# Kernel tuning notes

Hardware: AMD Instinct MI355X
Metric: run time of the kernel (lower is better)

Reference implementation:

```python
import jax, jax.numpy as jnp
import numpy as np

REG_MAX = 16
NC = 80
TOPK = 10
ALPHA = 0.5
BETA = 6.0
IMG = 640.0
EPS = 1e-7
BOX_W, CLS_W, DFL_W = 7.5, 0.5, 1.5


def make_anchors():
    anchors, strides = [], []
    for s, size in [(8, 80), (16, 40), (32, 20)]:
        yy, xx = jnp.meshgrid(jnp.arange(size, dtype=jnp.float32), jnp.arange(size, dtype=jnp.float32), indexing='ij')
        xy = (jnp.stack([xx, yy], -1).reshape(-1, 2) + 0.5) * s
        anchors.append(xy)
        strides.append(jnp.full((size * size,), float(s), jnp.float32))
    return jnp.concatenate(anchors), jnp.concatenate(strides)  # [A,2], [A]


def pairwise_iou(gt, pd, eps=EPS):
    # gt [B,G,4], pd [B,A,4] -> [B,G,A]
    b1 = gt[:, :, None, :]
    b2 = pd[:, None, :, :]
    inter = jnp.clip(jnp.minimum(b1[..., 2:], b2[..., 2:]) - jnp.maximum(b1[..., :2], b2[..., :2]), 0.0).prod(-1)
    a1 = (b1[..., 2:] - b1[..., :2]).prod(-1)
    a2 = (b2[..., 2:] - b2[..., :2]).prod(-1)
    return inter / (a1 + a2 - inter + eps)


def ciou(b1, b2, eps=EPS):
    # elementwise CIoU on [...,4] xyxy boxes
    inter = jnp.clip(jnp.minimum(b1[..., 2:], b2[..., 2:]) - jnp.maximum(b1[..., :2], b2[..., :2]), 0.0).prod(-1)
    area1 = jnp.maximum(b1[..., 2:] - b1[..., :2], eps).prod(-1)
    area2 = jnp.maximum(b2[..., 2:] - b2[..., :2], eps).prod(-1)
    union = area1 + area2 - inter + eps
    iou = inter / union
    cw = jnp.maximum(b1[..., 2], b2[..., 2]) - jnp.minimum(b1[..., 0], b2[..., 0])
    ch = jnp.maximum(b1[..., 3], b2[..., 3]) - jnp.minimum(b1[..., 1], b2[..., 1])
    c2 = cw * cw + ch * ch + eps
    c1c = (b1[..., :2] + b1[..., 2:]) * 0.5
    c2c = (b2[..., :2] + b2[..., 2:]) * 0.5
    rho2 = ((c1c - c2c) ** 2).sum(-1)
    w1 = jnp.maximum(b1[..., 2] - b1[..., 0], eps)
    h1 = jnp.maximum(b1[..., 3] - b1[..., 1], eps)
    w2 = jnp.maximum(b2[..., 2] - b2[..., 0], eps)
    h2 = jnp.maximum(b2[..., 3] - b2[..., 1], eps)
    v = (4.0 / jnp.pi ** 2) * (jnp.arctan(w2 / h2) - jnp.arctan(w1 / h1)) ** 2
    alpha = jax.lax.stop_gradient(v / (1.0 - iou + v + eps))
    return jnp.clip(iou - (rho2 / c2 + v * alpha), -1.0, 1.0)


def assign(pd_scores, pd_bboxes, gt_labels, gt_bboxes, mask_gt_f):
    # TaskAlignedAssigner.forward (runs under stop_gradient at call site)
    B, A, C = pd_scores.shape
    G = gt_bboxes.shape[1]
    iou = pairwise_iou(gt_bboxes, pd_bboxes)                       # [B,G,A]
    cls_score = pd_scores.max(-1)[:, None, :] * mask_gt_f[:, :, None]
    align = (cls_score ** ALPHA) * (iou ** BETA) * mask_gt_f[:, :, None]
    k = min(TOPK, A)
    vals, idx = jax.lax.top_k(align, k)                            # [B,G,k]
    valid = (mask_gt_f[:, :, None] > 0) & (vals > 0)
    b_ix = jnp.arange(B)[:, None, None]
    g_ix = jnp.arange(G)[None, :, None]
    mask_pos = jnp.zeros((B, G, A), bool).at[b_ix, g_ix, idx].max(valid)
    fg = mask_pos.any(1)                                           # [B,A]
    miou = iou * mask_pos.astype(iou.dtype)
    matched = miou.argmax(1)                                       # [B,A]
    tlab = jnp.take_along_axis(gt_labels, matched, 1)
    tlab = jnp.clip(tlab, 0, C - 1)
    tlab = jnp.where(fg, tlab, 0)
    tbox = jnp.take_along_axis(gt_bboxes, matched[..., None], 1)   # [B,A,4]
    iou_s = jnp.take_along_axis(miou, matched[:, None, :], 1)[:, 0, :]
    tscore = jax.nn.one_hot(tlab, C, dtype=pd_scores.dtype) * iou_s[..., None] * fg[..., None].astype(pd_scores.dtype)
    return tlab, tbox, tscore, fg


def yolo_loss(pred_dist, pred_cls, gt_labels, gt_bboxes, mask_gt):
    B, A, _ = pred_dist.shape
    R = REG_MAX
    anchors, strides = make_anchors()
    # decode: DFL expectation -> pixel boxes
    prob = jax.nn.softmax(pred_dist.reshape(B, A, 4, R), -1)
    dist = (prob * jnp.arange(R, dtype=prob.dtype)).sum(-1)        # stride units
    dpix = dist * strides[None, :, None]
    ax, ay = anchors[None, :, 0], anchors[None, :, 1]
    pred_boxes = jnp.clip(jnp.stack([ax - dpix[..., 0], ay - dpix[..., 1], ax + dpix[..., 2], ay + dpix[..., 3]], -1), 0.0, IMG)
    pd_scores = jax.nn.sigmoid(pred_cls)
    mgf = mask_gt.astype(jnp.float32)
    tlab, tbox, tscore, fg = jax.tree.map(jax.lax.stop_gradient, assign(pd_scores, pred_boxes, gt_labels, gt_bboxes, mgf))
    # cls: BCE with logits, sum / max(score_sum, 1)
    x, t = pred_cls, tscore
    bce = jnp.maximum(x, 0.0) - x * t + jnp.log1p(jnp.exp(-jnp.abs(x)))
    score_sum = jnp.maximum(tscore.sum(), 1.0)
    loss_cls = bce.sum() / score_sum
    fgf = fg.astype(jnp.float32)
    num_fg = jnp.maximum(fgf.sum(), 1.0)
    # box: mean(1 - CIoU) over foreground anchors
    loss_box = ((1.0 - ciou(pred_boxes, tbox)) * fgf).sum() / num_fg
    # DFL: box2dist in stride units, bilinear CE over left/right bins
    target_ltrb = jnp.stack([ax - tbox[..., 0], ay - tbox[..., 1], tbox[..., 2] - ax, tbox[..., 3] - ay], -1) / strides[None, :, None]
    target_ltrb = jnp.clip(target_ltrb, 0.0, R - 1.01)
    tleft = jnp.clip(jnp.floor(target_ltrb).astype(jnp.int32), 0, R - 1)
    tright = jnp.clip(tleft + 1, 0, R - 1)
    wr = jnp.clip(target_ltrb - tleft.astype(target_ltrb.dtype), 0.0, 1.0)
    wl = 1.0 - wr
    logp = jax.nn.log_softmax(pred_dist.reshape(B, A, 4, R), -1)
    ll = -jnp.take_along_axis(logp, tleft[..., None], -1)[..., 0]
    lr = -jnp.take_along_axis(logp, tright[..., None], -1)[..., 0]
    dfl = (ll * wl + lr * wr).sum(-1)                              # [B,A]
    loss_dfl = (dfl * fgf).sum() / num_fg / 4.0
    return BOX_W * loss_box + CLS_W * loss_cls + DFL_W * loss_dfl


def setup_inputs() -> dict:
    key = jax.random.key(0)
    k0, k1, k2, k3, k4 = jax.random.split(key, 5)
    B, A, G = 32, 8400, 40
    pred_dist = jax.random.normal(k0, (B, A, 4 * REG_MAX), dtype=jnp.float32)
    pred_cls = jax.random.normal(k1, (B, A, NC), dtype=jnp.float32)
    gt_labels = jax.random.randint(k2, (B, G), 0, NC)
    centers = jax.random.uniform(k3, (B, G, 2), minval=60.0, maxval=580.0)
    wh = jax.random.uniform(k4, (B, G, 2), minval=10.0, maxval=100.0)
    gt_bboxes = jnp.concatenate([centers - wh * 0.5, centers + wh * 0.5], -1).astype(jnp.float32)
    mask_gt = jnp.ones((B, G), dtype=bool)
    return {"pred_dist": pred_dist, "pred_cls": pred_cls, "gt_labels": gt_labels, "gt_bboxes": gt_bboxes, "mask_gt": mask_gt}


def reference(pred_dist, pred_cls, gt_labels, gt_bboxes, mask_gt):
    return yolo_loss(pred_dist, pred_cls, gt_labels, gt_bboxes, mask_gt)
```

## Files before the change

kernel.cpp:

```cpp
#include <hip/hip_runtime.h>
#include <cmath>


namespace {

constexpr int B = 32;
constexpr int A = 8400;
constexpr int G = 40;
constexpr int C = 80;
constexpr float EPS = 1e-7f;
constexpr float IMG = 640.0f;

constexpr int TPW = 16;
constexpr int NT = B * A / TPW;
constexpr int PRE_BLOCKS = 512;
constexpr int NWAVES = PRE_BLOCKS * 4;
constexpr int DIST_B = TPW * 64;
constexpr int CLS_B = TPW * 320;
constexpr int SLICE = DIST_B + CLS_B;

#define AS1 __attribute__((address_space(1)))
#define AS3 __attribute__((address_space(3)))

__device__ __forceinline__ void gload_lds16(const void* g, void* l) {
  __builtin_amdgcn_global_load_lds((AS1 void*)(g), (AS3 void*)(l), 16, 0, 0);
}

__device__ __forceinline__ void anchor_of(int a, float& ax, float& ay, float& st) {
  int x, y;
  if (a < 6400)      { x = a % 80; y = a / 80; st = 8.0f; }
  else if (a < 8000) { int t = a - 6400; x = t % 40; y = t / 40; st = 16.0f; }
  else               { int t = a - 8000; x = t % 20; y = t / 20; st = 32.0f; }
  ax = ((float)x + 0.5f) * st;
  ay = ((float)y + 0.5f) * st;
}

__device__ __forceinline__ void cls_part(const float4* c, float& sp, float& mx) {
  float relu = 0.f, p0 = 1.f, p1 = 1.f;
  mx = -3.4e38f;
#pragma unroll
  for (int q = 0; q < 5; ++q) {
    float xs[4] = {c[q].x, c[q].y, c[q].z, c[q].w};
#pragma unroll
    for (int e = 0; e < 4; ++e) {
      float x = xs[e];
      mx = fmaxf(mx, x);
      relu += fmaxf(x, 0.f);
      float ee = __expf(-fabsf(x));
      if (q < 3) p0 *= (1.f + ee); else p1 *= (1.f + ee);
    }
  }
  sp = relu + 0.69314718056f * (__log2f(p0) + __log2f(p1));
}

__device__ __forceinline__ float dist_expect(float4 w0, float4 w1, float4 w2, float4 w3) {
  float x[16] = {w0.x, w0.y, w0.z, w0.w, w1.x, w1.y, w1.z, w1.w,
                 w2.x, w2.y, w2.z, w2.w, w3.x, w3.y, w3.z, w3.w};
  float m = x[0];
#pragma unroll
  for (int e = 1; e < 16; ++e) m = fmaxf(m, x[e]);
  float se = 0.f, sj = 0.f;
#pragma unroll
  for (int e = 0; e < 16; ++e) {
    float ee = __expf(x[e] - m);
    se += ee;
    sj += ee * (float)e;
  }
  return sj / se;
}

__device__ __forceinline__ void stage_tile(const char* dbase, const char* cbase,
                                           int tile, char* lbuf, int lane) {
  const char* gd = dbase + (size_t)tile * DIST_B + lane * 16;
  const char* gc = cbase + (size_t)tile * CLS_B + lane * 16;
#pragma unroll
  for (int r = 0; r < 4; ++r) gload_lds16(gd + r * 1024, lbuf + r * 1024);
#pragma unroll
  for (int q = 0; q < 5; ++q) gload_lds16(gc + q * 1024, lbuf + DIST_B + q * 1024);
}

__global__ __launch_bounds__(256) void k_pre(
    const float* __restrict__ pred_dist, const float* __restrict__ pred_cls,
    float* __restrict__ pbox, float* __restrict__ msqrt,
    unsigned long long* __restrict__ mask, double* __restrict__ acc) {
  __shared__ char smem[4 * 2 * SLICE];
  __shared__ double shb[4];
  int t = threadIdx.x, lane = t & 63, wid = t >> 6;
  int j = lane & 3, a16 = lane >> 2;
  char* slice = smem + wid * (2 * SLICE);
  const char* dbase = (const char*)pred_dist;
  const char* cbase = (const char*)pred_cls;

  double spsum = 0.0;
  int cur = blockIdx.x * 4 + wid;
  int buf = 0;
  if (cur < NT) stage_tile(dbase, cbase, cur, slice, lane);

  while (cur < NT) {
    int nxt = cur + NWAVES;
    if (nxt < NT) {
      stage_tile(dbase, cbase, nxt, slice + (buf ^ 1) * SLICE, lane);
      __builtin_amdgcn_s_waitcnt(0xF79);
    } else {
      __builtin_amdgcn_s_waitcnt(0xF70);
    }

    const char* bp = slice + buf * SLICE;
    float4 c[5];
    const float4* cl = (const float4*)(bp + DIST_B + a16 * 320 + j * 16);
#pragma unroll
    for (int q = 0; q < 5; ++q) c[q] = cl[q * 4];
    float sp, mx;
    cls_part(c, sp, mx);
    mx = fmaxf(mx, __shfl_xor(mx, 1));
    mx = fmaxf(mx, __shfl_xor(mx, 2));

    const float4* dl = (const float4*)(bp + a16 * 256 + j * 64);
    float de = dist_expect(dl[0], dl[1], dl[2], dl[3]);
    int qb = lane & ~3;
    float e0 = __shfl(de, qb), e1 = __shfl(de, qb + 1);
    float e2 = __shfl(de, qb + 2), e3 = __shfl(de, qb + 3);

    int i = cur * TPW + a16;
    if (j == 0) {
      int a = i % A;
      float ax, ay, st;
      anchor_of(a, ax, ay, st);
      float4 ob;
      ob.x = fminf(fmaxf(ax - e0 * st, 0.f), IMG);
      ob.y = fminf(fmaxf(ay - e1 * st, 0.f), IMG);
      ob.z = fminf(fmaxf(ax + e2 * st, 0.f), IMG);
      ob.w = fminf(fmaxf(ay + e3 * st, 0.f), IMG);
      reinterpret_cast<float4*>(pbox)[i] = ob;
      msqrt[i] = sqrtf(1.f / (1.f + __expf(-mx)));
      mask[i] = 0ull;
    }
    spsum += (double)sp;
    cur = nxt;
    buf ^= 1;
  }

#pragma unroll
  for (int off = 32; off; off >>= 1) spsum += __shfl_xor(spsum, off);
  if (lane == 0) shb[wid] = spsum;
  __syncthreads();
  if (t == 0) {
    double s = shb[0] + shb[1] + shb[2] + shb[3];
    atomicAdd(&acc[0 * 8 + (blockIdx.x & 7)], s);
  }
}

__global__ __launch_bounds__(256) void k_topk(
    const float* __restrict__ pbox, const float* __restrict__ msqrt,
    const float* __restrict__ gt_bboxes, unsigned long long* __restrict__ mask) {
  int bg = blockIdx.x;
  int b = bg / G, g = bg % G;
  int t = threadIdx.x, lane = t & 63, wid = t >> 6;
  const float* gp = gt_bboxes + (size_t)bg * 4;
  float gx1 = gp[0], gy1 = gp[1], gx2 = gp[2], gy2 = gp[3];
  float garea = (gx2 - gx1) * (gy2 - gy1);
  const float4* pb = reinterpret_cast<const float4*>(pbox) + (size_t)b * A;
  const float* ms = msqrt + (size_t)b * A;

  float lv[10];
  int li[10];
#pragma unroll
  for (int s = 0; s < 10; ++s) { lv[s] = 0.f; li[s] = 0x7fffffff; }

  for (int a = t; a < A; a += 256) {
    float4 p = pb[a];
    float iw = fmaxf(fminf(gx2, p.z) - fmaxf(gx1, p.x), 0.f);
    float ih = fmaxf(fminf(gy2, p.w) - fmaxf(gy1, p.y), 0.f);
    float inter = iw * ih;
    float parea = (p.z - p.x) * (p.w - p.y);
    float iou = inter / (garea + parea - inter + EPS);
    float i2 = iou * iou;
    float v = ms[a] * i2 * i2 * i2;
    if (v > lv[9] || (v == lv[9] && v > 0.f && a < li[9])) {
      float cv = v; int ci = a;
#pragma unroll
      for (int s = 0; s < 10; ++s) {
        bool bt = (cv > lv[s]) || (cv == lv[s] && ci < li[s]);
        float tv = bt ? cv : lv[s]; int ti = bt ? ci : li[s];
        cv = bt ? lv[s] : cv; ci = bt ? li[s] : ci;
        lv[s] = tv; li[s] = ti;
      }
    }
  }

  __shared__ float swv[4];
  __shared__ int swi[4];
  __shared__ float sbv;
  __shared__ int sbi;
  int ptr = 0;
  unsigned long long* mrow = mask + (size_t)b * A;
  for (int k = 0; k < 10; ++k) {
    float hv = lv[0]; int hi = li[0];
#pragma unroll
    for (int s = 1; s < 10; ++s) { bool sel = (ptr == s); hv = sel ? lv[s] : hv; hi = sel ? li[s] : hi; }
    if (ptr > 9) { hv = -1.f; hi = -1; }
    float rv = hv; int ri = hi;
#pragma unroll
    for (int off = 32; off; off >>= 1) {
      float ov = __shfl_xor(rv, off); int oi = __shfl_xor(ri, off);
      if (ov > rv || (ov == rv && oi < ri)) { rv = ov; ri = oi; }
    }
    if (lane == 0) { swv[wid] = rv; swi[wid] = ri; }
    __syncthreads();
    if (t == 0) {
      float bv = swv[0]; int bi = swi[0];
#pragma unroll
      for (int w = 1; w < 4; ++w)
        if (swv[w] > bv || (swv[w] == bv && swi[w] < bi)) { bv = swv[w]; bi = swi[w]; }
      sbv = bv; sbi = bi;
      if (bv > 0.f) atomicOr(&mrow[bi], 1ull << g);
    }
    __syncthreads();
    if (sbv <= 0.f) break;
    if (hi == sbi) ptr++;
  }
}

__device__ __forceinline__ float ciou_f(float4 p, float t0, float t1, float t2, float t3) {
  float iw = fmaxf(fminf(p.z, t2) - fmaxf(p.x, t0), 0.f);
  float ih = fmaxf(fminf(p.w, t3) - fmaxf(p.y, t1), 0.f);
  float inter = iw * ih;
  float w1 = fmaxf(p.z - p.x, EPS), h1 = fmaxf(p.w - p.y, EPS);
  float w2 = fmaxf(t2 - t0, EPS), h2 = fmaxf(t3 - t1, EPS);
  float uni = w1 * h1 + w2 * h2 - inter + EPS;
  float iou = inter / uni;
  float cw = fmaxf(p.z, t2) - fminf(p.x, t0);
  float ch = fmaxf(p.w, t3) - fminf(p.y, t1);
  float c2 = cw * cw + ch * ch + EPS;
  float dx = (p.x + p.z) * 0.5f - (t0 + t2) * 0.5f;
  float dy = (p.y + p.w) * 0.5f - (t1 + t3) * 0.5f;
  float rho2 = dx * dx + dy * dy;
  float dat = atanf(w2 / h2) - atanf(w1 / h1);
  const float c4pi2 = (float)(4.0 / (M_PI * M_PI));
  float v = c4pi2 * dat * dat;
  float alpha = v / (1.0f - iou + v + EPS);
  float r = iou - (rho2 / c2 + v * alpha);
  return fminf(fmaxf(r, -1.f), 1.f);
}

__device__ __forceinline__ float wave_sum(float v) {
#pragma unroll
  for (int off = 32; off; off >>= 1) v += __shfl_xor(v, off);
  return v;
}

__global__ __launch_bounds__(256) void k_loss(
    const float* __restrict__ pred_dist, const float* __restrict__ pred_cls,
    const int* __restrict__ gt_labels, const float* __restrict__ gt_bboxes,
    const float* __restrict__ pbox, const unsigned long long* __restrict__ mask,
    double* __restrict__ acc) {
  int t = threadIdx.x, lane = t & 63, wid = t >> 6;
  int i = blockIdx.x * 256 + t;
  int b = i / A, a = i - b * A;
  unsigned long long mk = mask[i];
  float corr = 0.f, sc = 0.f, nfg = 0.f, box = 0.f, dfl = 0.f;
  if (mk) {
    float4 p = reinterpret_cast<const float4*>(pbox)[i];
    float parea = (p.z - p.x) * (p.w - p.y);
    float best = 0.f;
    int bestg = -1;
    unsigned long long mm = mk;
    while (mm) {
      int g = __ffsll((unsigned long long)mm) - 1;
      mm &= mm - 1;
      const float* gp = gt_bboxes + (size_t)(b * G + g) * 4;
      float gx1 = gp[0], gy1 = gp[1], gx2 = gp[2], gy2 = gp[3];
      float iw = fmaxf(fminf(gx2, p.z) - fmaxf(gx1, p.x), 0.f);
      float ih = fmaxf(fminf(gy2, p.w) - fmaxf(gy1, p.y), 0.f);
      float inter = iw * ih;
      float garea = (gx2 - gx1) * (gy2 - gy1);
      float iou = inter / (garea + parea - inter + EPS);
      if (iou > best) { best = iou; bestg = g; }
    }
    if (bestg >= 0) {
      sc = best;
      nfg = 1.f;
      int lab = gt_labels[b * G + bestg];
      lab = lab < 0 ? 0 : (lab > C - 1 ? C - 1 : lab);
      float xl = pred_cls[(size_t)i * C + lab];
      corr = -xl * best;
      const float* gp = gt_bboxes + (size_t)(b * G + bestg) * 4;
      float t0 = gp[0], t1 = gp[1], t2 = gp[2], t3 = gp[3];
      box = 1.0f - ciou_f(p, t0, t1, t2, t3);
      float ax, ay, st;
      anchor_of(a, ax, ay, st);
      float rst = 1.f / st;
      float tgt[4] = {(ax - t0) * rst, (ay - t1) * rst, (t2 - ax) * rst, (t3 - ay) * rst};
      const float4* dr = reinterpret_cast<const float4*>(pred_dist) + (size_t)i * 16;
      const float* drf = pred_dist + (size_t)i * 64;
#pragma unroll
      for (int l = 0; l < 4; ++l) {
        float4 u0 = dr[4 * l], u1 = dr[4 * l + 1], u2 = dr[4 * l + 2], u3 = dr[4 * l + 3];
        float xs[16] = {u0.x, u0.y, u0.z, u0.w, u1.x, u1.y, u1.z, u1.w,
                        u2.x, u2.y, u2.z, u2.w, u3.x, u3.y, u3.z, u3.w};
        float m = xs[0];
#pragma unroll
        for (int e = 1; e < 16; ++e) m = fmaxf(m, xs[e]);
        float se = 0.f;
#pragma unroll
        for (int e = 0; e < 16; ++e) se += __expf(xs[e] - m);
        float lse = m + __logf(se);
        float tt = fminf(fmaxf(tgt[l], 0.f), 14.99f);
        int tl = (int)tt;
        float wr = tt - (float)tl;
        float wl = 1.f - wr;
        float xa = drf[l * 16 + tl];
        float xb = drf[l * 16 + tl + 1];
        dfl += (lse - xa) * wl + (lse - xb) * wr;
      }
    }
  }
  float s0 = wave_sum(corr), s1 = wave_sum(sc), s2 = wave_sum(nfg);
  float s3 = wave_sum(box), s4 = wave_sum(dfl);
  __shared__ float sh[4][5];
  if (lane == 0) { sh[wid][0] = s0; sh[wid][1] = s1; sh[wid][2] = s2; sh[wid][3] = s3; sh[wid][4] = s4; }
  __syncthreads();
  if (t == 0) {
    double a0 = 0, a1 = 0, a2 = 0, a3 = 0, a4 = 0;
#pragma unroll
    for (int w = 0; w < 4; ++w) {
      a0 += sh[w][0]; a1 += sh[w][1]; a2 += sh[w][2]; a3 += sh[w][3]; a4 += sh[w][4];
    }
    if (a2 != 0.0) {
      int slot = blockIdx.x & 7;
      atomicAdd(&acc[0 * 8 + slot], a0);
      atomicAdd(&acc[1 * 8 + slot], a1);
      atomicAdd(&acc[2 * 8 + slot], a2);
      atomicAdd(&acc[3 * 8 + slot], a3);
      atomicAdd(&acc[4 * 8 + slot], a4);
    }
  }
}

__global__ void k_final(const double* __restrict__ acc, float* __restrict__ out) {
  double q[5];
#pragma unroll
  for (int jj = 0; jj < 5; ++jj) {
    double s = 0;
#pragma unroll
    for (int w = 0; w < 8; ++w) s += acc[jj * 8 + w];
    q[jj] = s;
  }
  double bce = q[0];
  double scs = fmax(q[1], 1.0);
  double nf = fmax(q[2], 1.0);
  double loss = 7.5 * (q[3] / nf) + 0.5 * (bce / scs) + 1.5 * (q[4] / nf / 4.0);
  out[0] = (float)loss;
}

}

extern "C" void kernel_launch(void* const* d_in, const int* in_sizes, int n_in,
                              void* d_out, int out_size, void* d_ws, size_t ws_size,
                              hipStream_t stream) {
  (void)in_sizes; (void)n_in; (void)out_size; (void)ws_size;
  const float* pred_dist = (const float*)d_in[0];
  const float* pred_cls  = (const float*)d_in[1];
  const int*   gt_labels = (const int*)d_in[2];
  const float* gt_bboxes = (const float*)d_in[3];

  unsigned long long* mask = (unsigned long long*)d_ws;
  double* acc  = (double*)((char*)d_ws + (size_t)B * A * 8);
  float*  pbox = (float*)((char*)d_ws + (size_t)B * A * 8 + 64 * 8);
  float*  msqrt = pbox + (size_t)B * A * 4;
  float*  out = (float*)d_out;

  hipMemsetAsync(acc, 0, 64 * 8, stream);
  hipLaunchKernelGGL(k_pre, dim3(PRE_BLOCKS), dim3(256), 0, stream,
                     pred_dist, pred_cls, pbox, msqrt, mask, acc);
  hipLaunchKernelGGL(k_topk, dim3(B * G), dim3(256), 0, stream,
                     pbox, msqrt, gt_bboxes, mask);
  hipLaunchKernelGGL(k_loss, dim3(B * A / 256), dim3(256), 0, stream,
                     pred_dist, pred_cls, gt_labels, gt_bboxes, pbox, mask, acc);
  hipLaunchKernelGGL(k_final, dim3(1), dim3(1), 0, stream, acc, out);
}
```

Measured before the change: 237.4 us.

## Fuse pre, topk, loss and final kernels into one cooperative kernel with grid syncs

Merges the four separate launches plus the memset into a single cooperative kernel of 512 blocks, with grid-wide syncs between the preprocessing, top-k assignment and loss phases. Per-block partial sums now go to arrays and are reduced deterministically by block 0, replacing the double atomics and the separate final kernel. This removes launch gaps and memset overhead. In exchange, the top-k phase runs on only 512 blocks looping over 1280 (b,g) pairs, and the loss phase loops over 1050 chunks, so these phases get less parallelism than before. The grid barriers also add their own cost.

```diff
diff --git a/kernel.cpp b/kernel.cpp
--- a/kernel.cpp
+++ b/kernel.cpp
@@ -1,5 +1,8 @@
 #include <hip/hip_runtime.h>
+#include <hip/hip_cooperative_groups.h>
 #include <cmath>
+
+namespace cg = cooperative_groups;
 
 
 namespace {
@@ -19,6 +22,8 @@
 constexpr int CLS_B = TPW * 320;
 constexpr int SLICE = DIST_B + CLS_B;
 
+constexpr int NLB = B * A / 256;
+
 #define AS1 __attribute__((address_space(1)))
 #define AS3 __attribute__((address_space(3)))
 
@@ -77,148 +82,6 @@
   for (int r = 0; r < 4; ++r) gload_lds16(gd + r * 1024, lbuf + r * 1024);
 #pragma unroll
   for (int q = 0; q < 5; ++q) gload_lds16(gc + q * 1024, lbuf + DIST_B + q * 1024);
-}
-
-__global__ __launch_bounds__(256) void k_pre(
-    const float* __restrict__ pred_dist, const float* __restrict__ pred_cls,
-    float* __restrict__ pbox, float* __restrict__ msqrt,
-    unsigned long long* __restrict__ mask, double* __restrict__ acc) {
-  __shared__ char smem[4 * 2 * SLICE];
-  __shared__ double shb[4];
-  int t = threadIdx.x, lane = t & 63, wid = t >> 6;
-  int j = lane & 3, a16 = lane >> 2;
-  char* slice = smem + wid * (2 * SLICE);
-  const char* dbase = (const char*)pred_dist;
-  const char* cbase = (const char*)pred_cls;
-
-  double spsum = 0.0;
-  int cur = blockIdx.x * 4 + wid;
-  int buf = 0;
-  if (cur < NT) stage_tile(dbase, cbase, cur, slice, lane);
-
-  while (cur < NT) {
-    int nxt = cur + NWAVES;
-    if (nxt < NT) {
-      stage_tile(dbase, cbase, nxt, slice + (buf ^ 1) * SLICE, lane);
-      __builtin_amdgcn_s_waitcnt(0xF79);
-    } else {
-      __builtin_amdgcn_s_waitcnt(0xF70);
-    }
-
-    const char* bp = slice + buf * SLICE;
-    float4 c[5];
-    const float4* cl = (const float4*)(bp + DIST_B + a16 * 320 + j * 16);
-#pragma unroll
-    for (int q = 0; q < 5; ++q) c[q] = cl[q * 4];
-    float sp, mx;
-    cls_part(c, sp, mx);
-    mx = fmaxf(mx, __shfl_xor(mx, 1));
-    mx = fmaxf(mx, __shfl_xor(mx, 2));
-
-    const float4* dl = (const float4*)(bp + a16 * 256 + j * 64);
-    float de = dist_expect(dl[0], dl[1], dl[2], dl[3]);
-    int qb = lane & ~3;
-    float e0 = __shfl(de, qb), e1 = __shfl(de, qb + 1);
-    float e2 = __shfl(de, qb + 2), e3 = __shfl(de, qb + 3);
-
-    int i = cur * TPW + a16;
-    if (j == 0) {
-      int a = i % A;
-      float ax, ay, st;
-      anchor_of(a, ax, ay, st);
-      float4 ob;
-      ob.x = fminf(fmaxf(ax - e0 * st, 0.f), IMG);
-      ob.y = fminf(fmaxf(ay - e1 * st, 0.f), IMG);
-      ob.z = fminf(fmaxf(ax + e2 * st, 0.f), IMG);
-      ob.w = fminf(fmaxf(ay + e3 * st, 0.f), IMG);
-      reinterpret_cast<float4*>(pbox)[i] = ob;
-      msqrt[i] = sqrtf(1.f / (1.f + __expf(-mx)));
-      mask[i] = 0ull;
-    }
-    spsum += (double)sp;
-    cur = nxt;
-    buf ^= 1;
-  }
-
-#pragma unroll
-  for (int off = 32; off; off >>= 1) spsum += __shfl_xor(spsum, off);
-  if (lane == 0) shb[wid] = spsum;
-  __syncthreads();
-  if (t == 0) {
-    double s = shb[0] + shb[1] + shb[2] + shb[3];
-    atomicAdd(&acc[0 * 8 + (blockIdx.x & 7)], s);
-  }
-}
-
-__global__ __launch_bounds__(256) void k_topk(
-    const float* __restrict__ pbox, const float* __restrict__ msqrt,
-    const float* __restrict__ gt_bboxes, unsigned long long* __restrict__ mask) {
-  int bg = blockIdx.x;
-  int b = bg / G, g = bg % G;
-  int t = threadIdx.x, lane = t & 63, wid = t >> 6;
-  const float* gp = gt_bboxes + (size_t)bg * 4;
-  float gx1 = gp[0], gy1 = gp[1], gx2 = gp[2], gy2 = gp[3];
-  float garea = (gx2 - gx1) * (gy2 - gy1);
-  const float4* pb = reinterpret_cast<const float4*>(pbox) + (size_t)b * A;
-  const float* ms = msqrt + (size_t)b * A;
-
-  float lv[10];
-  int li[10];
-#pragma unroll
-  for (int s = 0; s < 10; ++s) { lv[s] = 0.f; li[s] = 0x7fffffff; }
-
-  for (int a = t; a < A; a += 256) {
-    float4 p = pb[a];
-    float iw = fmaxf(fminf(gx2, p.z) - fmaxf(gx1, p.x), 0.f);
-    float ih = fmaxf(fminf(gy2, p.w) - fmaxf(gy1, p.y), 0.f);
-    float inter = iw * ih;
-    float parea = (p.z - p.x) * (p.w - p.y);
-    float iou = inter / (garea + parea - inter + EPS);
-    float i2 = iou * iou;
-    float v = ms[a] * i2 * i2 * i2;
-    if (v > lv[9] || (v == lv[9] && v > 0.f && a < li[9])) {
-      float cv = v; int ci = a;
-#pragma unroll
-      for (int s = 0; s < 10; ++s) {
-        bool bt = (cv > lv[s]) || (cv == lv[s] && ci < li[s]);
-        float tv = bt ? cv : lv[s]; int ti = bt ? ci : li[s];
-        cv = bt ? lv[s] : cv; ci = bt ? li[s] : ci;
-        lv[s] = tv; li[s] = ti;
-      }
-    }
-  }
-
-  __shared__ float swv[4];
-  __shared__ int swi[4];
-  __shared__ float sbv;
-  __shared__ int sbi;
-  int ptr = 0;
-  unsigned long long* mrow = mask + (size_t)b * A;
-  for (int k = 0; k < 10; ++k) {
-    float hv = lv[0]; int hi = li[0];
-#pragma unroll
-    for (int s = 1; s < 10; ++s) { bool sel = (ptr == s); hv = sel ? lv[s] : hv; hi = sel ? li[s] : hi; }
-    if (ptr > 9) { hv = -1.f; hi = -1; }
-    float rv = hv; int ri = hi;
-#pragma unroll
-    for (int off = 32; off; off >>= 1) {
-      float ov = __shfl_xor(rv, off); int oi = __shfl_xor(ri, off);
-      if (ov > rv || (ov == rv && oi < ri)) { rv = ov; ri = oi; }
-    }
-    if (lane == 0) { swv[wid] = rv; swi[wid] = ri; }
-    __syncthreads();
-    if (t == 0) {
-      float bv = swv[0]; int bi = swi[0];
-#pragma unroll
-      for (int w = 1; w < 4; ++w)
-        if (swv[w] > bv || (swv[w] == bv && swi[w] < bi)) { bv = swv[w]; bi = swi[w]; }
-      sbv = bv; sbi = bi;
-      if (bv > 0.f) atomicOr(&mrow[bi], 1ull << g);
-    }
-    __syncthreads();
-    if (sbv <= 0.f) break;
-    if (hi == sbi) ptr++;
-  }
 }
 
 __device__ __forceinline__ float ciou_f(float4 p, float t0, float t1, float t2, float t3) {
@@ -249,108 +112,265 @@
   return v;
 }
 
-__global__ __launch_bounds__(256) void k_loss(
+__device__ __forceinline__ double wave_sum_d(double v) {
+#pragma unroll
+  for (int off = 32; off; off >>= 1) v += __shfl_xor(v, off);
+  return v;
+}
+
+__global__ __launch_bounds__(256, 2) void k_fused(
     const float* __restrict__ pred_dist, const float* __restrict__ pred_cls,
     const int* __restrict__ gt_labels, const float* __restrict__ gt_bboxes,
-    const float* __restrict__ pbox, const unsigned long long* __restrict__ mask,
-    double* __restrict__ acc) {
+    float* __restrict__ pbox, float* __restrict__ msqrt,
+    unsigned long long* __restrict__ mask,
+    double* __restrict__ preacc, double* __restrict__ lacc,
+    float* __restrict__ out) {
+  cg::grid_group gg = cg::this_grid();
+
+  __shared__ char smem[4 * 2 * SLICE];
+  __shared__ double shb[4];
+  __shared__ float swv[4];
+  __shared__ int swi[4];
+  __shared__ float sbv;
+  __shared__ int sbi;
+  __shared__ float shl[4][5];
+  __shared__ double fin[4][6];
+
   int t = threadIdx.x, lane = t & 63, wid = t >> 6;
-  int i = blockIdx.x * 256 + t;
-  int b = i / A, a = i - b * A;
-  unsigned long long mk = mask[i];
-  float corr = 0.f, sc = 0.f, nfg = 0.f, box = 0.f, dfl = 0.f;
-  if (mk) {
-    float4 p = reinterpret_cast<const float4*>(pbox)[i];
-    float parea = (p.z - p.x) * (p.w - p.y);
-    float best = 0.f;
-    int bestg = -1;
-    unsigned long long mm = mk;
-    while (mm) {
-      int g = __ffsll((unsigned long long)mm) - 1;
-      mm &= mm - 1;
-      const float* gp = gt_bboxes + (size_t)(b * G + g) * 4;
-      float gx1 = gp[0], gy1 = gp[1], gx2 = gp[2], gy2 = gp[3];
+
+  {
+    int j = lane & 3, a16 = lane >> 2;
+    char* slice = smem + wid * (2 * SLICE);
+    const char* dbase = (const char*)pred_dist;
+    const char* cbase = (const char*)pred_cls;
+
+    double spsum = 0.0;
+    int cur = blockIdx.x * 4 + wid;
+    int buf = 0;
+    if (cur < NT) stage_tile(dbase, cbase, cur, slice, lane);
+
+    while (cur < NT) {
+      int nxt = cur + NWAVES;
+      if (nxt < NT) {
+        stage_tile(dbase, cbase, nxt, slice + (buf ^ 1) * SLICE, lane);
+        __builtin_amdgcn_s_waitcnt(0xF79);
+      } else {
+        __builtin_amdgcn_s_waitcnt(0xF70);
+      }
+
+      const char* bp = slice + buf * SLICE;
+      float4 c[5];
+      const float4* cl = (const float4*)(bp + DIST_B + a16 * 320 + j * 16);
+#pragma unroll
+      for (int q = 0; q < 5; ++q) c[q] = cl[q * 4];
+      float sp, mx;
+      cls_part(c, sp, mx);
+      mx = fmaxf(mx, __shfl_xor(mx, 1));
+      mx = fmaxf(mx, __shfl_xor(mx, 2));
+
+      const float4* dl = (const float4*)(bp + a16 * 256 + j * 64);
+      float de = dist_expect(dl[0], dl[1], dl[2], dl[3]);
+      int qb = lane & ~3;
+      float e0 = __shfl(de, qb), e1 = __shfl(de, qb + 1);
+      float e2 = __shfl(de, qb + 2), e3 = __shfl(de, qb + 3);
+
+      int i = cur * TPW + a16;
+      if (j == 0) {
+        int a = i % A;
+        float ax, ay, st;
+        anchor_of(a, ax, ay, st);
+        float4 ob;
+        ob.x = fminf(fmaxf(ax - e0 * st, 0.f), IMG);
+        ob.y = fminf(fmaxf(ay - e1 * st, 0.f), IMG);
+        ob.z = fminf(fmaxf(ax + e2 * st, 0.f), IMG);
+        ob.w = fminf(fmaxf(ay + e3 * st, 0.f), IMG);
+        reinterpret_cast<float4*>(pbox)[i] = ob;
+        msqrt[i] = sqrtf(1.f / (1.f + __expf(-mx)));
+        mask[i] = 0ull;
+      }
+      spsum += (double)sp;
+      cur = nxt;
+      buf ^= 1;
+    }
+
+#pragma unroll
+    for (int off = 32; off; off >>= 1) spsum += __shfl_xor(spsum, off);
+    if (lane == 0) shb[wid] = spsum;
+    __syncthreads();
+    if (t == 0) preacc[blockIdx.x] = shb[0] + shb[1] + shb[2] + shb[3];
+  }
+
+  gg.sync();
+
+  for (int bg = blockIdx.x; bg < B * G; bg += PRE_BLOCKS) {
+    __syncthreads();
+    int b = bg / G, g = bg % G;
+    const float* gp = gt_bboxes + (size_t)bg * 4;
+    float gx1 = gp[0], gy1 = gp[1], gx2 = gp[2], gy2 = gp[3];
+    float garea = (gx2 - gx1) * (gy2 - gy1);
+    const float4* pb = reinterpret_cast<const float4*>(pbox) + (size_t)b * A;
+    const float* ms = msqrt + (size_t)b * A;
+
+    float lv[10];
+    int li[10];
+#pragma unroll
+    for (int s = 0; s < 10; ++s) { lv[s] = 0.f; li[s] = 0x7fffffff; }
+
+    for (int a = t; a < A; a += 256) {
+      float4 p = pb[a];
       float iw = fmaxf(fminf(gx2, p.z) - fmaxf(gx1, p.x), 0.f);
       float ih = fmaxf(fminf(gy2, p.w) - fmaxf(gy1, p.y), 0.f);
       float inter = iw * ih;
-      float garea = (gx2 - gx1) * (gy2 - gy1);
+      float parea = (p.z - p.x) * (p.w - p.y);
       float iou = inter / (garea + parea - inter + EPS);
-      if (iou > best) { best = iou; bestg = g; }
-    }
-    if (bestg >= 0) {
-      sc = best;
-      nfg = 1.f;
-      int lab = gt_labels[b * G + bestg];
-      lab = lab < 0 ? 0 : (lab > C - 1 ? C - 1 : lab);
-      float xl = pred_cls[(size_t)i * C + lab];
-      corr = -xl * best;
-      const float* gp = gt_bboxes + (size_t)(b * G + bestg) * 4;
-      float t0 = gp[0], t1 = gp[1], t2 = gp[2], t3 = gp[3];
-      box = 1.0f - ciou_f(p, t0, t1, t2, t3);
-      float ax, ay, st;
-      anchor_of(a, ax, ay, st);
-      float rst = 1.f / st;
-      float tgt[4] = {(ax - t0) * rst, (ay - t1) * rst, (t2 - ax) * rst, (t3 - ay) * rst};
-      const float4* dr = reinterpret_cast<const float4*>(pred_dist) + (size_t)i * 16;
-      const float* drf = pred_dist + (size_t)i * 64;
-#pragma unroll
-      for (int l = 0; l < 4; ++l) {
-        float4 u0 = dr[4 * l], u1 = dr[4 * l + 1], u2 = dr[4 * l + 2], u3 = dr[4 * l + 3];
-        float xs[16] = {u0.x, u0.y, u0.z, u0.w, u1.x, u1.y, u1.z, u1.w,
-                        u2.x, u2.y, u2.z, u2.w, u3.x, u3.y, u3.z, u3.w};
-        float m = xs[0];
-#pragma unroll
-        for (int e = 1; e < 16; ++e) m = fmaxf(m, xs[e]);
-        float se = 0.f;
-#pragma unroll
-        for (int e = 0; e < 16; ++e) se += __expf(xs[e] - m);
-        float lse = m + __logf(se);
-        float tt = fminf(fmaxf(tgt[l], 0.f), 14.99f);
-        int tl = (int)tt;
-        float wr = tt - (float)tl;
-        float wl = 1.f - wr;
-        float xa = drf[l * 16 + tl];
-        float xb = drf[l * 16 + tl + 1];
-        dfl += (lse - xa) * wl + (lse - xb) * wr;
-      }
-    }
-  }
-  float s0 = wave_sum(corr), s1 = wave_sum(sc), s2 = wave_sum(nfg);
-  float s3 = wave_sum(box), s4 = wave_sum(dfl);
-  __shared__ float sh[4][5];
-  if (lane == 0) { sh[wid][0] = s0; sh[wid][1] = s1; sh[wid][2] = s2; sh[wid][3] = s3; sh[wid][4] = s4; }
-  __syncthreads();
-  if (t == 0) {
-    double a0 = 0, a1 = 0, a2 = 0, a3 = 0, a4 = 0;
-#pragma unroll
-    for (int w = 0; w < 4; ++w) {
-      a0 += sh[w][0]; a1 += sh[w][1]; a2 += sh[w][2]; a3 += sh[w][3]; a4 += sh[w][4];
-    }
-    if (a2 != 0.0) {
-      int slot = blockIdx.x & 7;
-      atomicAdd(&acc[0 * 8 + slot], a0);
-      atomicAdd(&acc[1 * 8 + slot], a1);
-      atomicAdd(&acc[2 * 8 + slot], a2);
-      atomicAdd(&acc[3 * 8 + slot], a3);
-      atomicAdd(&acc[4 * 8 + slot], a4);
-    }
-  }
-}
-
-__global__ void k_final(const double* __restrict__ acc, float* __restrict__ out) {
-  double q[5];
-#pragma unroll
-  for (int jj = 0; jj < 5; ++jj) {
-    double s = 0;
-#pragma unroll
-    for (int w = 0; w < 8; ++w) s += acc[jj * 8 + w];
-    q[jj] = s;
-  }
-  double bce = q[0];
-  double scs = fmax(q[1], 1.0);
-  double nf = fmax(q[2], 1.0);
-  double loss = 7.5 * (q[3] / nf) + 0.5 * (bce / scs) + 1.5 * (q[4] / nf / 4.0);
-  out[0] = (float)loss;
+      float i2 = iou * iou;
+      float v = ms[a] * i2 * i2 * i2;
+      if (v > lv[9] || (v == lv[9] && v > 0.f && a < li[9])) {
+        float cv = v; int ci = a;
+#pragma unroll
+        for (int s = 0; s < 10; ++s) {
+          bool bt = (cv > lv[s]) || (cv == lv[s] && ci < li[s]);
+          float tv = bt ? cv : lv[s]; int ti = bt ? ci : li[s];
+          cv = bt ? lv[s] : cv; ci = bt ? li[s] : ci;
+          lv[s] = tv; li[s] = ti;
+        }
+      }
+    }
+
+    int ptr = 0;
+    unsigned long long* mrow = mask + (size_t)b * A;
+    for (int k = 0; k < 10; ++k) {
+      float hv = lv[0]; int hi = li[0];
+#pragma unroll
+      for (int s = 1; s < 10; ++s) { bool sel = (ptr == s); hv = sel ? lv[s] : hv; hi = sel ? li[s] : hi; }
+      if (ptr > 9) { hv = -1.f; hi = -1; }
+      float rv = hv; int ri = hi;
+#pragma unroll
+      for (int off = 32; off; off >>= 1) {
+        float ov = __shfl_xor(rv, off); int oi = __shfl_xor(ri, off);
+        if (ov > rv || (ov == rv && oi < ri)) { rv = ov; ri = oi; }
+      }
+      if (lane == 0) { swv[wid] = rv; swi[wid] = ri; }
+      __syncthreads();
+      if (t == 0) {
+        float bv = swv[0]; int bi = swi[0];
+#pragma unroll
+        for (int w = 1; w < 4; ++w)
+          if (swv[w] > bv || (swv[w] == bv && swi[w] < bi)) { bv = swv[w]; bi = swi[w]; }
+        sbv = bv; sbi = bi;
+        if (bv > 0.f) atomicOr(&mrow[bi], 1ull << g);
+      }
+      __syncthreads();
+      if (sbv <= 0.f) break;
+      if (hi == sbi) ptr++;
+    }
+  }
+
+  gg.sync();
+
+  for (int chunk = blockIdx.x; chunk < NLB; chunk += PRE_BLOCKS) {
+    __syncthreads();
+    int i = chunk * 256 + t;
+    int b = i / A, a = i - b * A;
+    unsigned long long mk = mask[i];
+    float corr = 0.f, sc = 0.f, nfg = 0.f, box = 0.f, dfl = 0.f;
+    if (mk) {
+      float4 p = reinterpret_cast<const float4*>(pbox)[i];
+      float parea = (p.z - p.x) * (p.w - p.y);
+      float best = 0.f;
+      int bestg = -1;
+      unsigned long long mm = mk;
+      while (mm) {
+        int g = __ffsll((unsigned long long)mm) - 1;
+        mm &= mm - 1;
+        const float* gp = gt_bboxes + (size_t)(b * G + g) * 4;
+        float gx1 = gp[0], gy1 = gp[1], gx2 = gp[2], gy2 = gp[3];
+        float iw = fmaxf(fminf(gx2, p.z) - fmaxf(gx1, p.x), 0.f);
+        float ih = fmaxf(fminf(gy2, p.w) - fmaxf(gy1, p.y), 0.f);
+        float inter = iw * ih;
+        float garea = (gx2 - gx1) * (gy2 - gy1);
+        float iou = inter / (garea + parea - inter + EPS);
+        if (iou > best) { best = iou; bestg = g; }
+      }
+      if (bestg >= 0) {
+        sc = best;
+        nfg = 1.f;
+        int lab = gt_labels[b * G + bestg];
+        lab = lab < 0 ? 0 : (lab > C - 1 ? C - 1 : lab);
+        float xl = pred_cls[(size_t)i * C + lab];
+        corr = -xl * best;
+        const float* gp = gt_bboxes + (size_t)(b * G + bestg) * 4;
+        float t0 = gp[0], t1 = gp[1], t2 = gp[2], t3 = gp[3];
+        box = 1.0f - ciou_f(p, t0, t1, t2, t3);
+        float ax, ay, st;
+        anchor_of(a, ax, ay, st);
+        float rst = 1.f / st;
+        float tgt[4] = {(ax - t0) * rst, (ay - t1) * rst, (t2 - ax) * rst, (t3 - ay) * rst};
+        const float4* dr = reinterpret_cast<const float4*>(pred_dist) + (size_t)i * 16;
+        const float* drf = pred_dist + (size_t)i * 64;
+#pragma unroll
+        for (int l = 0; l < 4; ++l) {
+          float4 u0 = dr[4 * l], u1 = dr[4 * l + 1], u2 = dr[4 * l + 2], u3 = dr[4 * l + 3];
+          float xs[16] = {u0.x, u0.y, u0.z, u0.w, u1.x, u1.y, u1.z, u1.w,
+                          u2.x, u2.y, u2.z, u2.w, u3.x, u3.y, u3.z, u3.w};
+          float m = xs[0];
+#pragma unroll
+          for (int e = 1; e < 16; ++e) m = fmaxf(m, xs[e]);
+          float se = 0.f;
+#pragma unroll
+          for (int e = 0; e < 16; ++e) se += __expf(xs[e] - m);
+          float lse = m + __logf(se);
+          float tt = fminf(fmaxf(tgt[l], 0.f), 14.99f);
+          int tl = (int)tt;
+          float wr = tt - (float)tl;
+          float wl = 1.f - wr;
+          float xa = drf[l * 16 + tl];
+          float xb = drf[l * 16 + tl + 1];
+          dfl += (lse - xa) * wl + (lse - xb) * wr;
+        }
+      }
+    }
+    float s0 = wave_sum(corr), s1 = wave_sum(sc), s2 = wave_sum(nfg);
+    float s3 = wave_sum(box), s4 = wave_sum(dfl);
+    if (lane == 0) { shl[wid][0] = s0; shl[wid][1] = s1; shl[wid][2] = s2; shl[wid][3] = s3; shl[wid][4] = s4; }
+    __syncthreads();
+    if (t == 0) {
+      double a0 = 0, a1 = 0, a2 = 0, a3 = 0, a4 = 0;
+#pragma unroll
+      for (int w = 0; w < 4; ++w) {
+        a0 += shl[w][0]; a1 += shl[w][1]; a2 += shl[w][2]; a3 += shl[w][3]; a4 += shl[w][4];
+      }
+      double* s = lacc + (size_t)chunk * 5;
+      s[0] = a0; s[1] = a1; s[2] = a2; s[3] = a3; s[4] = a4;
+    }
+  }
+
+  gg.sync();
+
+  if (blockIdx.x == 0) {
+    double q0 = 0, q1 = 0, q2 = 0, q3 = 0, q4 = 0, q5 = 0;
+    for (int c = t; c < NLB; c += 256) {
+      const double* s = lacc + (size_t)c * 5;
+      q0 += s[0]; q1 += s[1]; q2 += s[2]; q3 += s[3]; q4 += s[4];
+    }
+    for (int c = t; c < PRE_BLOCKS; c += 256) q5 += preacc[c];
+    q0 = wave_sum_d(q0); q1 = wave_sum_d(q1); q2 = wave_sum_d(q2);
+    q3 = wave_sum_d(q3); q4 = wave_sum_d(q4); q5 = wave_sum_d(q5);
+    if (lane == 0) {
+      fin[wid][0] = q0; fin[wid][1] = q1; fin[wid][2] = q2;
+      fin[wid][3] = q3; fin[wid][4] = q4; fin[wid][5] = q5;
+    }
+    __syncthreads();
+    if (t == 0) {
+      double Q[6];
+#pragma unroll
+      for (int z = 0; z < 6; ++z) Q[z] = fin[0][z] + fin[1][z] + fin[2][z] + fin[3][z];
+      double bce = Q[0] + Q[5];
+      double scs = fmax(Q[1], 1.0);
+      double nf = fmax(Q[2], 1.0);
+      out[0] = (float)(7.5 * (Q[3] / nf) + 0.5 * (bce / scs) + 1.5 * (Q[4] / nf / 4.0));
+    }
+  }
 }
 
 }
@@ -365,17 +385,14 @@
   const float* gt_bboxes = (const float*)d_in[3];
 
   unsigned long long* mask = (unsigned long long*)d_ws;
-  double* acc  = (double*)((char*)d_ws + (size_t)B * A * 8);
-  float*  pbox = (float*)((char*)d_ws + (size_t)B * A * 8 + 64 * 8);
-  float*  msqrt = pbox + (size_t)B * A * 4;
-  float*  out = (float*)d_out;
-
-  hipMemsetAsync(acc, 0, 64 * 8, stream);
-  hipLaunchKernelGGL(k_pre, dim3(PRE_BLOCKS), dim3(256), 0, stream,
-                     pred_dist, pred_cls, pbox, msqrt, mask, acc);
-  hipLaunchKernelGGL(k_topk, dim3(B * G), dim3(256), 0, stream,
-                     pbox, msqrt, gt_bboxes, mask);
-  hipLaunchKernelGGL(k_loss, dim3(B * A / 256), dim3(256), 0, stream,
-                     pred_dist, pred_cls, gt_labels, gt_bboxes, pbox, mask, acc);
-  hipLaunchKernelGGL(k_final, dim3(1), dim3(1), 0, stream, acc, out);
-}
+  float*  pbox   = (float*)((char*)d_ws + (size_t)B * A * 8);
+  float*  msqrt  = pbox + (size_t)B * A * 4;
+  double* preacc = (double*)((char*)d_ws + (size_t)B * A * 8 + (size_t)B * A * 16 + (size_t)B * A * 4);
+  double* lacc   = preacc + PRE_BLOCKS;
+  float*  out    = (float*)d_out;
+
+  void* args[] = {&pred_dist, &pred_cls, &gt_labels, &gt_bboxes,
+                  &pbox, &msqrt, &mask, &preacc, &lacc, &out};
+  hipLaunchCooperativeKernel((const void*)k_fused, dim3(PRE_BLOCKS), dim3(256),
+                             args, 0, stream);
+}
```

After: 435.2 us. +83.4%, slower.

## Pack best-IoU and GT index via atomicMax, fuse final reduction into loss kernel

Applied to the files above, without the earlier changes.

Instead of building a per-anchor GT bitmask and rescanning every set bit in the loss kernel to find the best IoU, the top-k kernel computes the IoU and uses a 64-bit atomicMax on a packed (iou bits, 63-g) word. The loss kernel then decodes the best GT directly. The memset and the separate final kernel are removed: accumulators are zeroed in the top-k kernel, k_pre writes per-block partial sums, and the last loss block (found with a counter) does the final reduction. This cuts two launches and the bitmask loop, but tie-breaking now depends on float bit ordering and the zeroing relies on k_topk finishing before k_loss starts.

```diff
diff --git a/kernel.cpp b/kernel.cpp
--- a/kernel.cpp
+++ b/kernel.cpp
@@ -19,6 +19,8 @@
 constexpr int CLS_B = TPW * 320;
 constexpr int SLICE = DIST_B + CLS_B;
 
+constexpr int NLB = B * A / 256;
+
 #define AS1 __attribute__((address_space(1)))
 #define AS3 __attribute__((address_space(3)))
 
@@ -82,7 +84,7 @@
 __global__ __launch_bounds__(256) void k_pre(
     const float* __restrict__ pred_dist, const float* __restrict__ pred_cls,
     float* __restrict__ pbox, float* __restrict__ msqrt,
-    unsigned long long* __restrict__ mask, double* __restrict__ acc) {
+    unsigned long long* __restrict__ packed, double* __restrict__ preacc) {
   __shared__ char smem[4 * 2 * SLICE];
   __shared__ double shb[4];
   int t = threadIdx.x, lane = t & 63, wid = t >> 6;
@@ -133,7 +135,7 @@
       ob.w = fminf(fmaxf(ay + e3 * st, 0.f), IMG);
       reinterpret_cast<float4*>(pbox)[i] = ob;
       msqrt[i] = sqrtf(1.f / (1.f + __expf(-mx)));
-      mask[i] = 0ull;
+      packed[i] = 0ull;
     }
     spsum += (double)sp;
     cur = nxt;
@@ -144,18 +146,20 @@
   for (int off = 32; off; off >>= 1) spsum += __shfl_xor(spsum, off);
   if (lane == 0) shb[wid] = spsum;
   __syncthreads();
-  if (t == 0) {
-    double s = shb[0] + shb[1] + shb[2] + shb[3];
-    atomicAdd(&acc[0 * 8 + (blockIdx.x & 7)], s);
-  }
+  if (t == 0) preacc[blockIdx.x] = shb[0] + shb[1] + shb[2] + shb[3];
 }
 
 __global__ __launch_bounds__(256) void k_topk(
     const float* __restrict__ pbox, const float* __restrict__ msqrt,
-    const float* __restrict__ gt_bboxes, unsigned long long* __restrict__ mask) {
+    const float* __restrict__ gt_bboxes, unsigned long long* __restrict__ packed,
+    double* __restrict__ acc, unsigned int* __restrict__ cnt) {
   int bg = blockIdx.x;
+  int t = threadIdx.x, lane = t & 63, wid = t >> 6;
+  if (bg == 0) {
+    if (t < 48) acc[t] = 0.0;
+    else if (t == 48) *cnt = 0u;
+  }
   int b = bg / G, g = bg % G;
-  int t = threadIdx.x, lane = t & 63, wid = t >> 6;
   const float* gp = gt_bboxes + (size_t)bg * 4;
   float gx1 = gp[0], gy1 = gp[1], gx2 = gp[2], gy2 = gp[3];
   float garea = (gx2 - gx1) * (gy2 - gy1);
@@ -193,7 +197,6 @@
   __shared__ float sbv;
   __shared__ int sbi;
   int ptr = 0;
-  unsigned long long* mrow = mask + (size_t)b * A;
   for (int k = 0; k < 10; ++k) {
     float hv = lv[0]; int hi = li[0];
 #pragma unroll
@@ -213,7 +216,17 @@
       for (int w = 1; w < 4; ++w)
         if (swv[w] > bv || (swv[w] == bv && swi[w] < bi)) { bv = swv[w]; bi = swi[w]; }
       sbv = bv; sbi = bi;
-      if (bv > 0.f) atomicOr(&mrow[bi], 1ull << g);
+      if (bv > 0.f) {
+        float4 p = pb[bi];
+        float iw = fmaxf(fminf(gx2, p.z) - fmaxf(gx1, p.x), 0.f);
+        float ih = fmaxf(fminf(gy2, p.w) - fmaxf(gy1, p.y), 0.f);
+        float inter = iw * ih;
+        float parea = (p.z - p.x) * (p.w - p.y);
+        float iou = inter / (garea + parea - inter + EPS);
+        unsigned long long pk =
+            ((unsigned long long)__float_as_uint(iou) << 32) | (unsigned int)(63 - g);
+        atomicMax(&packed[(size_t)b * A + bi], pk);
+      }
     }
     __syncthreads();
     if (sbv <= 0.f) break;
@@ -249,75 +262,69 @@
   return v;
 }
 
+__device__ __forceinline__ double wave_sum_d(double v) {
+#pragma unroll
+  for (int off = 32; off; off >>= 1) v += __shfl_xor(v, off);
+  return v;
+}
+
 __global__ __launch_bounds__(256) void k_loss(
     const float* __restrict__ pred_dist, const float* __restrict__ pred_cls,
     const int* __restrict__ gt_labels, const float* __restrict__ gt_bboxes,
-    const float* __restrict__ pbox, const unsigned long long* __restrict__ mask,
-    double* __restrict__ acc) {
+    const float* __restrict__ pbox, const unsigned long long* __restrict__ packed,
+    double* __restrict__ acc, const double* __restrict__ preacc,
+    unsigned int* __restrict__ cnt, float* __restrict__ out) {
   int t = threadIdx.x, lane = t & 63, wid = t >> 6;
   int i = blockIdx.x * 256 + t;
   int b = i / A, a = i - b * A;
-  unsigned long long mk = mask[i];
+  unsigned long long pk = packed[i];
   float corr = 0.f, sc = 0.f, nfg = 0.f, box = 0.f, dfl = 0.f;
-  if (mk) {
+  if (pk) {
+    int bestg = 63 - (int)(pk & 63ull);
+    float best = __uint_as_float((unsigned int)(pk >> 32));
     float4 p = reinterpret_cast<const float4*>(pbox)[i];
-    float parea = (p.z - p.x) * (p.w - p.y);
-    float best = 0.f;
-    int bestg = -1;
-    unsigned long long mm = mk;
-    while (mm) {
-      int g = __ffsll((unsigned long long)mm) - 1;
-      mm &= mm - 1;
-      const float* gp = gt_bboxes + (size_t)(b * G + g) * 4;
-      float gx1 = gp[0], gy1 = gp[1], gx2 = gp[2], gy2 = gp[3];
-      float iw = fmaxf(fminf(gx2, p.z) - fmaxf(gx1, p.x), 0.f);
-      float ih = fmaxf(fminf(gy2, p.w) - fmaxf(gy1, p.y), 0.f);
-      float inter = iw * ih;
-      float garea = (gx2 - gx1) * (gy2 - gy1);
-      float iou = inter / (garea + parea - inter + EPS);
-      if (iou > best) { best = iou; bestg = g; }
-    }
-    if (bestg >= 0) {
-      sc = best;
-      nfg = 1.f;
-      int lab = gt_labels[b * G + bestg];
-      lab = lab < 0 ? 0 : (lab > C - 1 ? C - 1 : lab);
-      float xl = pred_cls[(size_t)i * C + lab];
-      corr = -xl * best;
-      const float* gp = gt_bboxes + (size_t)(b * G + bestg) * 4;
-      float t0 = gp[0], t1 = gp[1], t2 = gp[2], t3 = gp[3];
-      box = 1.0f - ciou_f(p, t0, t1, t2, t3);
-      float ax, ay, st;
-      anchor_of(a, ax, ay, st);
-      float rst = 1.f / st;
-      float tgt[4] = {(ax - t0) * rst, (ay - t1) * rst, (t2 - ax) * rst, (t3 - ay) * rst};
-      const float4* dr = reinterpret_cast<const float4*>(pred_dist) + (size_t)i * 16;
-      const float* drf = pred_dist + (size_t)i * 64;
-#pragma unroll
-      for (int l = 0; l < 4; ++l) {
-        float4 u0 = dr[4 * l], u1 = dr[4 * l + 1], u2 = dr[4 * l + 2], u3 = dr[4 * l + 3];
-        float xs[16] = {u0.x, u0.y, u0.z, u0.w, u1.x, u1.y, u1.z, u1.w,
-                        u2.x, u2.y, u2.z, u2.w, u3.x, u3.y, u3.z, u3.w};
-        float m = xs[0];
-#pragma unroll
-        for (int e = 1; e < 16; ++e) m = fmaxf(m, xs[e]);
-        float se = 0.f;
-#pragma unroll
-        for (int e = 0; e < 16; ++e) se += __expf(xs[e] - m);
-        float lse = m + __logf(se);
-        float tt = fminf(fmaxf(tgt[l], 0.f), 14.99f);
-        int tl = (int)tt;
-        float wr = tt - (float)tl;
-        float wl = 1.f - wr;
-        float xa = drf[l * 16 + tl];
-        float xb = drf[l * 16 + tl + 1];
-        dfl += (lse - xa) * wl + (lse - xb) * wr;
-      }
+    sc = best;
+    nfg = 1.f;
+    int lab = gt_labels[b * G + bestg];
+    lab = lab < 0 ? 0 : (lab > C - 1 ? C - 1 : lab);
+    float xl = pred_cls[(size_t)i * C + lab];
+    corr = -xl * best;
+    const float* gp = gt_bboxes + (size_t)(b * G + bestg) * 4;
+    float t0 = gp[0], t1 = gp[1], t2 = gp[2], t3 = gp[3];
+    box = 1.0f - ciou_f(p, t0, t1, t2, t3);
+    float ax, ay, st;
+    anchor_of(a, ax, ay, st);
+    float rst = 1.f / st;
+    float tgt[4] = {(ax - t0) * rst, (ay - t1) * rst, (t2 - ax) * rst, (t3 - ay) * rst};
+    const float4* dr = reinterpret_cast<const float4*>(pred_dist) + (size_t)i * 16;
+    const float* drf = pred_dist + (size_t)i * 64;
+#pragma unroll
+    for (int l = 0; l < 4; ++l) {
+      float4 u0 = dr[4 * l], u1 = dr[4 * l + 1], u2 = dr[4 * l + 2], u3 = dr[4 * l + 3];
+      float xs[16] = {u0.x, u0.y, u0.z, u0.w, u1.x, u1.y, u1.z, u1.w,
+                      u2.x, u2.y, u2.z, u2.w, u3.x, u3.y, u3.z, u3.w};
+      float m = xs[0];
+#pragma unroll
+      for (int e = 1; e < 16; ++e) m = fmaxf(m, xs[e]);
+      float se = 0.f;
+#pragma unroll
+      for (int e = 0; e < 16; ++e) se += __expf(xs[e] - m);
+      float lse = m + __logf(se);
+      float tt = fminf(fmaxf(tgt[l], 0.f), 14.99f);
+      int tl = (int)tt;
+      float wr = tt - (float)tl;
+      float wl = 1.f - wr;
+      float xa = drf[l * 16 + tl];
+      float xb = drf[l * 16 + tl + 1];
+      dfl += (lse - xa) * wl + (lse - xb) * wr;
     }
   }
   float s0 = wave_sum(corr), s1 = wave_sum(sc), s2 = wave_sum(nfg);
   float s3 = wave_sum(box), s4 = wave_sum(dfl);
   __shared__ float sh[4][5];
+  __shared__ double sq[4];
+  __shared__ double sacc[40];
+  __shared__ int isLast;
   if (lane == 0) { sh[wid][0] = s0; sh[wid][1] = s1; sh[wid][2] = s2; sh[wid][3] = s3; sh[wid][4] = s4; }
   __syncthreads();
   if (t == 0) {
@@ -334,23 +341,33 @@
       atomicAdd(&acc[3 * 8 + slot], a3);
       atomicAdd(&acc[4 * 8 + slot], a4);
     }
-  }
-}
-
-__global__ void k_final(const double* __restrict__ acc, float* __restrict__ out) {
-  double q[5];
-#pragma unroll
-  for (int jj = 0; jj < 5; ++jj) {
-    double s = 0;
-#pragma unroll
-    for (int w = 0; w < 8; ++w) s += acc[jj * 8 + w];
-    q[jj] = s;
-  }
-  double bce = q[0];
-  double scs = fmax(q[1], 1.0);
-  double nf = fmax(q[2], 1.0);
-  double loss = 7.5 * (q[3] / nf) + 0.5 * (bce / scs) + 1.5 * (q[4] / nf / 4.0);
-  out[0] = (float)loss;
+    __threadfence();
+    unsigned int old = atomicAdd(cnt, 1u);
+    isLast = (old == (unsigned int)(NLB - 1)) ? 1 : 0;
+  }
+  __syncthreads();
+  if (isLast) {
+    double q5 = 0.0;
+    for (int c = t; c < PRE_BLOCKS; c += 256) q5 += preacc[c];
+    q5 = wave_sum_d(q5);
+    if (lane == 0) sq[wid] = q5;
+    if (t < 40) sacc[t] = atomicAdd(&acc[t], 0.0);
+    __syncthreads();
+    if (t == 0) {
+      double Q[5];
+#pragma unroll
+      for (int j5 = 0; j5 < 5; ++j5) {
+        double s = 0.0;
+#pragma unroll
+        for (int w = 0; w < 8; ++w) s += sacc[j5 * 8 + w];
+        Q[j5] = s;
+      }
+      double bce = Q[0] + sq[0] + sq[1] + sq[2] + sq[3];
+      double scs = fmax(Q[1], 1.0);
+      double nf = fmax(Q[2], 1.0);
+      out[0] = (float)(7.5 * (Q[3] / nf) + 0.5 * (bce / scs) + 1.5 * (Q[4] / nf / 4.0));
+    }
+  }
 }
 
 }
@@ -364,18 +381,19 @@
   const int*   gt_labels = (const int*)d_in[2];
   const float* gt_bboxes = (const float*)d_in[3];
 
-  unsigned long long* mask = (unsigned long long*)d_ws;
-  double* acc  = (double*)((char*)d_ws + (size_t)B * A * 8);
-  float*  pbox = (float*)((char*)d_ws + (size_t)B * A * 8 + 64 * 8);
+  unsigned long long* packed = (unsigned long long*)d_ws;
+  double* acc   = (double*)((char*)d_ws + (size_t)B * A * 8);
+  unsigned int* cnt = (unsigned int*)((char*)acc + 48 * 8);
+  float*  pbox  = (float*)((char*)acc + 64 * 8);
   float*  msqrt = pbox + (size_t)B * A * 4;
-  float*  out = (float*)d_out;
-
-  hipMemsetAsync(acc, 0, 64 * 8, stream);
+  double* preacc = (double*)(msqrt + (size_t)B * A);
+  float*  out   = (float*)d_out;
+
   hipLaunchKernelGGL(k_pre, dim3(PRE_BLOCKS), dim3(256), 0, stream,
-                     pred_dist, pred_cls, pbox, msqrt, mask, acc);
+                     pred_dist, pred_cls, pbox, msqrt, packed, preacc);
   hipLaunchKernelGGL(k_topk, dim3(B * G), dim3(256), 0, stream,
-                     pbox, msqrt, gt_bboxes, mask);
+                     pbox, msqrt, gt_bboxes, packed, acc, cnt);
   hipLaunchKernelGGL(k_loss, dim3(B * A / 256), dim3(256), 0, stream,
-                     pred_dist, pred_cls, gt_labels, gt_bboxes, pbox, mask, acc);
-  hipLaunchKernelGGL(k_final, dim3(1), dim3(1), 0, stream, acc, out);
-}
+                     pred_dist, pred_cls, gt_labels, gt_bboxes, pbox, packed,
+                     acc, preacc, cnt, out);
+}
```

Result: slower. 247.2 us (+4.1%).
